# Kernel tuning notes

Hardware: AMD Instinct MI355X
Metric: run time of the kernel (lower is better)

## Reference

```python
import jax, jax.numpy as jnp
import numpy as np

B, T, H = 16, 512, 768
S = 32            # gold spans per example
L = 50            # max_span_len -> candidate ends per span
NT = 3            # num_types
HS = 4 * H        # span repr size


def setup_inputs() -> dict:
    key = jax.random.key(0)
    ks = jax.random.split(key, 8)
    h = jax.random.normal(ks[0], (B, T, H), dtype=jnp.float32)
    attention_mask = jnp.ones((B, T), dtype=jnp.int32)
    starts = jax.random.randint(ks[1], (B, S), 1, 400).astype(jnp.int32)
    lens = jax.random.randint(ks[2], (B, S), 0, L).astype(jnp.int32)
    ends = starts + lens                      # <= 448 < last_tok=510
    types = jax.random.randint(ks[3], (B, S), 0, NT).astype(jnp.int32)
    W1 = jax.random.normal(ks[4], (HS, HS), dtype=jnp.float32) * (1.0 / np.sqrt(HS))
    b1 = jnp.zeros((HS,), dtype=jnp.float32)
    w_score = jax.random.normal(ks[5], (HS,), dtype=jnp.float32) * (1.0 / np.sqrt(HS))
    b_score = jnp.zeros((1,), dtype=jnp.float32)
    W_type = jax.random.normal(ks[6], (HS, NT), dtype=jnp.float32) * (1.0 / np.sqrt(HS))
    b_type = jnp.zeros((NT,), dtype=jnp.float32)
    return {"h": h, "attention_mask": attention_mask, "span_starts": starts,
            "span_ends": ends, "span_types": types, "W1": W1, "b1": b1,
            "w_score": w_score, "b_score": b_score, "W_type": W_type, "b_type": b_type}


def _span_loss(h, attention_mask, span_starts, span_ends, span_types,
               W1, b1, w_score, b_score, W_type, b_type, type_loss_weight=1.0):
    cls = h[:, 0]                                              # [B,H]
    # prefix sums for O(1) segment means: pre[b,t] = sum h[b,0:t]
    pre = jnp.concatenate([jnp.zeros((B, 1, H), h.dtype), jnp.cumsum(h, axis=1)], axis=1)

    valid_len = attention_mask.sum(axis=1)                     # [B]
    last_tok = jnp.maximum(1, valid_len - 2)                   # [B]

    s = span_starts                                            # [B,S]
    e_gold = span_ends
    gold_idx = e_gold - s                                      # [B,S]
    lt = last_tok[:, None]
    span_valid = (s >= 1) & (s <= lt) & (e_gold >= s) & (e_gold <= lt) & (gold_idx < L)

    e_max = jnp.minimum(s + L - 1, lt)                         # [B,S]
    p = s[..., None] + jnp.arange(L, dtype=s.dtype)            # [B,S,L] candidate ends
    cand_valid = p <= e_max[..., None]

    sc = jnp.clip(s, 0, T - 1)
    pc = jnp.clip(p, 0, T - 1)
    bi2 = jnp.arange(B)[:, None]
    bi3 = jnp.arange(B)[:, None, None]

    h_start = h[bi2, sc]                                       # [B,S,H]
    h_end = h[bi3, pc]                                         # [B,S,L,H]
    seg_len = jnp.maximum(p - s[..., None] + 1, 1).astype(h.dtype)
    h_mean = (pre[bi3, pc + 1] - pre[bi2, sc][:, :, None]) / seg_len[..., None]

    repr_ = jnp.concatenate([
        jnp.broadcast_to(h_start[:, :, None], (B, S, L, H)),
        h_end,
        h_mean,
        jnp.broadcast_to(cls[:, None, None], (B, S, L, H)),
    ], axis=-1)                                                # [B,S,L,4H]

    h1 = jax.nn.gelu(jnp.einsum('bslh,hd->bsld', repr_, W1) + b1, approximate=False)
    scores = jnp.einsum('bsld,d->bsl', h1, w_score) + b_score[0]      # [B,S,L]
    type_logits = jnp.einsum('bsld,dk->bslk', h1, W_type) + b_type    # [B,S,L,NT]

    # end-index CE over valid candidate ends
    masked = jnp.where(cand_valid, scores, jnp.float32(-1e9))
    logp_end = jax.nn.log_softmax(masked, axis=-1)             # [B,S,L]
    gi = jnp.clip(gold_idx, 0, L - 1)
    end_loss = -jnp.take_along_axis(logp_end, gi[..., None], axis=-1)[..., 0]  # [B,S]

    # type CE at the gold end index
    tl_gold = jnp.take_along_axis(type_logits, gi[..., None, None], axis=2)[:, :, 0]  # [B,S,NT]
    logp_t = jax.nn.log_softmax(tl_gold, axis=-1)
    tg = jnp.clip(span_types, 0, NT - 1)
    type_loss = -jnp.take_along_axis(logp_t, tg[..., None], axis=-1)[..., 0]  # [B,S]

    vmask = span_valid.astype(h.dtype)
    n_seg = vmask.sum()
    denom = jnp.maximum(n_seg, 1.0)
    loss_end = jnp.where(n_seg > 0, (end_loss * vmask).sum() / denom, 0.0)
    loss_type = jnp.where(n_seg > 0, (type_loss * vmask).sum() / denom, 0.0)
    return loss_end + type_loss_weight * loss_type


def reference(h, attention_mask, span_starts, span_ends, span_types,
              W1, b1, w_score, b_score, W_type, b_type):
    return _span_loss(h, attention_mask, span_starts, span_ends, span_types,
                      W1, b1, w_score, b_score, W_type, b_type)
```

## Files before the change

kernel.cpp:

```cpp
#include <hip/hip_runtime.h>
#include <hip/hip_bf16.h>
#include <math.h>

#define B_ 16
#define T_ 512
#define H_ 768
#define S_ 32
#define L_ 50
#define NT_ 3
#define HS_ 3072
#define CH_ 32
#define CT_ 16

#define TX_ 464
#define YB2 7424
#define GB 14848
#define CLSB 15360
#define XYROWS 14848
#define AROWS 15616
#define NKT 24
#define SLOT_SH 16384

typedef __attribute__((ext_vector_type(8))) short short8;
typedef __attribute__((ext_vector_type(4))) float f32x4;

__device__ __forceinline__ unsigned short f2bf(float f) {
    __hip_bfloat16 b = __float2bfloat16(f);
    return *(unsigned short*)&b;
}
__device__ __forceinline__ float bf2f(unsigned short u) {
    union { unsigned int i; float f; } v; v.i = ((unsigned int)u) << 16; return v.f;
}
__device__ __forceinline__ void load_lds16(const void* g, void* l) {
    __builtin_amdgcn_global_load_lds((__attribute__((address_space(1))) void*)g,
                                     (__attribute__((address_space(3))) void*)l, 16, 0, 0);
}
__device__ __forceinline__ ushort4 pack4(float4 v) {
    ushort4 o; o.x = f2bf(v.x); o.y = f2bf(v.y); o.z = f2bf(v.z); o.w = f2bf(v.w);
    return o;
}

__device__ __forceinline__ float gelu_exact(float v) {
    float a = fabsf(v) * 0.70710678118654752f;
    float t = __builtin_amdgcn_rcpf(fmaf(a, 0.47047f, 1.0f));
    float poly = t * fmaf(t, fmaf(t, 0.7478556f, -0.0958798f), 0.3480242f);
    float e = __builtin_amdgcn_exp2f(a * a * -1.4426950408889634f);
    float erfa = fmaf(-poly, e, 1.0f);
    float erfv = copysignf(erfa, v);
    return 0.5f * v * (1.0f + erfv);
}

__global__ __launch_bounds__(256) void cumsum_pass1(const float4* __restrict__ h4,
                                                    float4* __restrict__ partial) {
    int idx = blockIdx.x * 256 + threadIdx.x;
    int hd4 = idx % 192; int t = idx / 192; int ch = t % CH_; int b = t / CH_;
    const float4* hp = h4 + ((size_t)b * T_ + ch * CT_) * 192 + hd4;
    float4 acc = {0.f, 0.f, 0.f, 0.f};
#pragma unroll
    for (int tt = 0; tt < CT_; tt++) {
        float4 v = hp[(size_t)tt * 192];
        acc.x += v.x; acc.y += v.y; acc.z += v.z; acc.w += v.w;
    }
    partial[idx] = acc;
}

__global__ __launch_bounds__(256) void cumsum_pass3(const float4* __restrict__ h4,
                                                    const float4* __restrict__ partial,
                                                    ushort4* __restrict__ Ab4,
                                                    const float* __restrict__ h,
                                                    const int* __restrict__ starts) {
    if (blockIdx.x >= B_ * CH_ * 192 / 256) {
        int r = blockIdx.x - B_ * CH_ * 192 / 256;
        int src_row, dst_row;
        if (r < B_ * S_) {
            int b = r / S_;
            int sv = starts[r];
            int sc = min(max(sv, 0), T_ - 1);
            src_row = b * T_ + sc;
            dst_row = GB + r;
        } else {
            int b = r - B_ * S_;
            src_row = b * T_;
            dst_row = CLSB + b;
        }
        __hip_bfloat16* dst = (__hip_bfloat16*)Ab4 + (size_t)dst_row * H_;
        const float* src = h + (size_t)src_row * H_;
        for (int j = threadIdx.x; j < H_; j += 256)
            dst[j] = __float2bfloat16(src[j]);
        return;
    }
    int idx = blockIdx.x * 256 + threadIdx.x;
    int hd4 = idx % 192; int t = idx / 192; int ch = t % CH_; int b = t / CH_;
    if (ch * CT_ >= TX_) return;
    float4 acc = {0.f, 0.f, 0.f, 0.f};
#pragma unroll
    for (int c = 0; c < CH_; c++) {
        if (c < ch) {
            float4 v = partial[((size_t)b * CH_ + c) * 192 + hd4];
            acc.x += v.x; acc.y += v.y; acc.z += v.z; acc.w += v.w;
        }
    }
    const float4* hp = h4 + ((size_t)b * T_ + ch * CT_) * 192 + hd4;
    if (ch == 0) {
        ushort4 z = {0, 0, 0, 0};
        Ab4[((size_t)(YB2 + b * TX_)) * 192 + hd4] = z;
    }
#pragma unroll
    for (int tt = 0; tt < CT_; tt++) {
        int t2 = ch * CT_ + tt;
        float4 hv = hp[(size_t)tt * 192];
        if (t2 < TX_)
            Ab4[((size_t)(b * TX_ + t2)) * 192 + hd4] = pack4(hv);
        acc.x += hv.x; acc.y += hv.y; acc.z += hv.z; acc.w += hv.w;
        if (t2 + 1 < TX_)
            Ab4[((size_t)(YB2 + b * TX_ + t2 + 1)) * 192 + hd4] = pack4(acc);
    }
}

__global__ __launch_bounds__(256) void transpose_w(const float* __restrict__ W1,
                                                   __hip_bfloat16* __restrict__ Wt) {
    __shared__ float tile[64][65];
    int n0 = blockIdx.x * 64, k0 = blockIdx.y * 64;
    int c = threadIdx.x & 63, r0 = threadIdx.x >> 6;
#pragma unroll
    for (int i = 0; i < 16; i++) {
        int r = r0 + i * 4;
        tile[r][c] = W1[(size_t)(k0 + r) * HS_ + n0 + c];
    }
    __syncthreads();
    int p = k0 / H_, kl = k0 % H_;
    __hip_bfloat16* out = Wt + (size_t)p * HS_ * H_;
#pragma unroll
    for (int i = 0; i < 16; i++) {
        int r = r0 + i * 4;
        out[(size_t)(n0 + r) * H_ + kl + c] = __float2bfloat16(tile[c][r]);
    }
}

__device__ __forceinline__ void mfma16(const short8 (&a)[4], const short8 (&b)[4],
                                       f32x4 (&acc)[8][4], int off) {
#pragma unroll
    for (int mf = 0; mf < 4; ++mf)
#pragma unroll
        for (int nf = 0; nf < 4; ++nf)
            acc[off + mf][nf] = __builtin_amdgcn_mfma_f32_16x16x32_bf16(
                a[mf], b[nf], acc[off + mf][nf], 0, 0, 0);
}

#define STAGE_A(nslot, k0_) {                                                  \
    char* d_ = (char*)(nslot) + dstoff;                                        \
    load_lds16(pA + (k0_), d_);                                                \
    load_lds16(pA + (size_t)128 * H_ + (k0_), d_ + 8192);                      \
}
#define STAGE_B(nslot, k0_) {                                                  \
    char* d_ = (char*)(nslot) + 16384 + dstoff;                                \
    load_lds16(pB + (k0_), d_);                                                \
    load_lds16(pB + (size_t)128 * H_ + (k0_), d_ + 8192);                      \
}

#define TILE_STEP(kt, WAITSTR, DO_STAGE)                                       \
  {                                                                            \
    const short* slot = lds + ((kt) & 3) * SLOT_SH;                            \
    short* nslot = lds + (((kt) + 3) & 3) * SLOT_SH;                           \
    asm volatile(WAITSTR ::: "memory");                                        \
    __builtin_amdgcn_s_barrier();                                              \
    __builtin_amdgcn_sched_barrier(0);                                         \
    short8 a[4], b[4];                                                         \
    _Pragma("unroll")                                                          \
    for (int i = 0; i < 4; ++i)                                                \
      a[i] = *(const short8*)&slot[(wr * 128 + i * 16 + l15) * 32 + pcs];      \
    _Pragma("unroll")                                                          \
    for (int i = 0; i < 4; ++i)                                                \
      b[i] = *(const short8*)&slot[8192 + (wc * 64 + i * 16 + l15) * 32 + pcs];\
    if (DO_STAGE) { STAGE_A(nslot, ((kt) + 3) * 32) }                          \
    asm volatile("s_waitcnt lgkmcnt(0)" ::: "memory");                         \
    __builtin_amdgcn_sched_barrier(0);                                         \
    __builtin_amdgcn_s_setprio(1);                                             \
    mfma16(a, b, acc, 0);                                                      \
    __builtin_amdgcn_s_setprio(0);                                             \
    __builtin_amdgcn_s_barrier();                                              \
    _Pragma("unroll")                                                          \
    for (int i = 0; i < 4; ++i)                                                \
      a[i] = *(const short8*)&slot[(wr * 128 + 64 + i * 16 + l15) * 32 + pcs]; \
    if (DO_STAGE) { STAGE_B(nslot, ((kt) + 3) * 32) }                          \
    asm volatile("s_waitcnt lgkmcnt(0)" ::: "memory");                         \
    __builtin_amdgcn_sched_barrier(0);                                         \
    __builtin_amdgcn_s_setprio(1);                                             \
    mfma16(a, b, acc, 4);                                                      \
    __builtin_amdgcn_s_setprio(0);                                             \
  }

__global__ __launch_bounds__(512, 2) void mfma_gemm(const __hip_bfloat16* __restrict__ Ab,
                                                    const __hip_bfloat16* __restrict__ Wt,
                                                    __hip_bfloat16* __restrict__ XY,
                                                    float* __restrict__ ST,
                                                    float* __restrict__ CC) {
    __shared__ short lds[4 * SLOT_SH];
    int tid = threadIdx.x;
    int wave = tid >> 6, lane = tid & 63;
    int wr = wave >> 2, wc = wave & 3;
    int l15 = lane & 15;
    int pcs = ((lane >> 4) ^ ((l15 >> 1) & 3)) * 8;

    int orig = blockIdx.x;
    int xcd = orig & 7, loc = orig >> 3;
    int wg = (xcd < 4 ? xcd * 92 : 368 + (xcd - 4) * 91) + loc;
    int mt = wg / 12, nt = wg - mt * 12;
    int m0 = mt << 8, n0 = nt << 8;

    const __hip_bfloat16* Bt;
    if (m0 < YB2)        Bt = Wt + (size_t)1 * HS_ * H_;
    else if (m0 < GB)    Bt = Wt + (size_t)2 * HS_ * H_;
    else if (m0 < CLSB)  Bt = Wt;
    else                 Bt = Wt + (size_t)3 * HS_ * H_;

    int srow = wave * 16 + (lane >> 2);
    int lcS = ((lane & 3) ^ ((lane >> 3) & 3)) * 8;
    const __hip_bfloat16* pA = Ab + (size_t)(m0 + srow) * H_ + lcS;
    const __hip_bfloat16* pB = Bt + (size_t)(n0 + srow) * H_ + lcS;
    int dstoff = wave * 1024;

    f32x4 acc[8][4] = {};

#pragma unroll
    for (int t = 0; t < 3; ++t) {
        STAGE_A(lds + t * SLOT_SH, t * 32)
        STAGE_B(lds + t * SLOT_SH, t * 32)
    }

    for (int kt = 0; kt < NKT - 3; ++kt)
        TILE_STEP(kt, "s_waitcnt vmcnt(8)", true)
    TILE_STEP(NKT - 3, "s_waitcnt vmcnt(8)", false)
    TILE_STEP(NKT - 2, "s_waitcnt vmcnt(4)", false)
    TILE_STEP(NKT - 1, "s_waitcnt vmcnt(0)", false)

    int mb = m0 + wr * 128, nb = n0 + wc * 64;
#pragma unroll
    for (int mf = 0; mf < 8; ++mf) {
#pragma unroll
        for (int nf = 0; nf < 4; ++nf) {
            int n = nb + nf * 16 + l15;
            int mr = mb + mf * 16 + (lane >> 4) * 4;
#pragma unroll
            for (int r = 0; r < 4; ++r) {
                int m = mr + r;
                float v = acc[mf][nf][r];
                if (m < XYROWS) {
                    XY[(size_t)m * HS_ + n] = __float2bfloat16(v);
                } else if (m < CLSB) {
                    ST[(size_t)(m - GB) * HS_ + n] = v;
                } else if (m < CLSB + 16) {
                    CC[(size_t)(m - CLSB) * HS_ + n] = v;
                }
            }
        }
    }
}

__global__ __launch_bounds__(256) void combine_kernel(
    const float* __restrict__ ST, const float* __restrict__ CC,
    const float* __restrict__ b1, const float* __restrict__ w_score,
    const __hip_bfloat16* __restrict__ XY,
    const float* __restrict__ b_score, const float* __restrict__ W_type,
    const int* __restrict__ starts, const int* __restrict__ ends,
    float* __restrict__ scores, float* __restrict__ tgold) {
    int x = blockIdx.x;
    int b = x & 15, s = x >> 4;
    int bs = b * S_ + s;
    int wave = threadIdx.x >> 6, lane = threadIdx.x & 63;
    int sv = starts[bs], ev = ends[bs];
    int gi = min(max(ev - sv, 0), L_ - 1);
    int sc = min(max(sv, 0), TX_ - 1);
    float bs0 = b_score[0];

    union U8 { short8 s; unsigned short u[8]; };
    short8 ysv[6], cv[6], wv[6];
    const unsigned short* Ysr = (const unsigned short*)(XY + (size_t)(YB2 + b * TX_ + sc) * HS_);
    const float* STr = ST + (size_t)bs * HS_;
    const float* CCr = CC + (size_t)b * HS_;
#pragma unroll
    for (int j = 0; j < 6; j++) {
        int d = j * 512 + lane * 8;
        ysv[j] = *(const short8*)(Ysr + d);
        float4 sa = *(const float4*)(STr + d),     sb = *(const float4*)(STr + d + 4);
        float4 ca = *(const float4*)(CCr + d),     cb = *(const float4*)(CCr + d + 4);
        float4 ba = *(const float4*)(b1 + d),      bb = *(const float4*)(b1 + d + 4);
        U8 uc;
        uc.u[0] = f2bf(sa.x + ca.x + ba.x); uc.u[1] = f2bf(sa.y + ca.y + ba.y);
        uc.u[2] = f2bf(sa.z + ca.z + ba.z); uc.u[3] = f2bf(sa.w + ca.w + ba.w);
        uc.u[4] = f2bf(sb.x + cb.x + bb.x); uc.u[5] = f2bf(sb.y + cb.y + bb.y);
        uc.u[6] = f2bf(sb.z + cb.z + bb.z); uc.u[7] = f2bf(sb.w + cb.w + bb.w);
        cv[j] = uc.s;
        float4 wa = *(const float4*)(w_score + d), wb = *(const float4*)(w_score + d + 4);
        U8 uw;
        uw.u[0] = f2bf(wa.x); uw.u[1] = f2bf(wa.y); uw.u[2] = f2bf(wa.z); uw.u[3] = f2bf(wa.w);
        uw.u[4] = f2bf(wb.x); uw.u[5] = f2bf(wb.y); uw.u[6] = f2bf(wb.z); uw.u[7] = f2bf(wb.w);
        wv[j] = uw.s;
    }

    for (int pr = wave; pr < L_ / 2; pr += 4) {
        int l0 = pr * 2, l1 = l0 + 1;
        int pc0 = min(max(sv + l0, 0), TX_ - 2);
        int pc1 = min(max(sv + l1, 0), TX_ - 2);
        float inv0 = 1.0f / (float)(l0 + 1);
        float inv1 = 1.0f / (float)(l1 + 1);
        bool isg0 = (l0 == gi), isg1 = (l1 == gi);
        bool anyg = isg0 || isg1;

        const unsigned short* X0 = (const unsigned short*)(XY + (size_t)(b * TX_ + pc0) * HS_);
        const unsigned short* X1 = (const unsigned short*)(XY + (size_t)(b * TX_ + pc1) * HS_);
        const unsigned short* Y0 = (const unsigned short*)(XY + (size_t)(YB2 + b * TX_ + pc0 + 1) * HS_);
        const unsigned short* Y1 = (const unsigned short*)(XY + (size_t)(YB2 + b * TX_ + pc1 + 1) * HS_);

        float local0 = 0.f, local1 = 0.f, t0 = 0.f, t1 = 0.f, t2 = 0.f;
#pragma unroll
        for (int j = 0; j < 6; j++) {
            int d = j * 512 + lane * 8;
            short8 xv0 = *(const short8*)(X0 + d);
            short8 xv1 = *(const short8*)(X1 + d);
            short8 yv0 = *(const short8*)(Y0 + d);
            short8 yv1 = *(const short8*)(Y1 + d);
#pragma unroll
            for (int q = 0; q < 8; q++) {
                float ys = bf2f(((const unsigned short*)&ysv[j])[q]);
                float cvq = bf2f(((const unsigned short*)&cv[j])[q]);
                float w  = bf2f(((const unsigned short*)&wv[j])[q]);
                float v0 = fmaf(bf2f(((const unsigned short*)&yv0)[q]) - ys, inv0, cvq) +
                           bf2f(((const unsigned short*)&xv0)[q]);
                float v1 = fmaf(bf2f(((const unsigned short*)&yv1)[q]) - ys, inv1, cvq) +
                           bf2f(((const unsigned short*)&xv1)[q]);
                float g0 = gelu_exact(v0);
                float g1 = gelu_exact(v1);
                local0 = fmaf(g0, w, local0);
                local1 = fmaf(g1, w, local1);
                if (anyg) {
                    float gg = isg0 ? g0 : g1;
                    t0 = fmaf(gg, W_type[(d + q) * NT_ + 0], t0);
                    t1 = fmaf(gg, W_type[(d + q) * NT_ + 1], t1);
                    t2 = fmaf(gg, W_type[(d + q) * NT_ + 2], t2);
                }
            }
        }
#pragma unroll
        for (int off = 32; off >= 1; off >>= 1) {
            local0 += __shfl_down(local0, off);
            local1 += __shfl_down(local1, off);
        }
        if (lane == 0) {
            scores[(size_t)bs * L_ + l0] = local0 + bs0;
            scores[(size_t)bs * L_ + l1] = local1 + bs0;
        }
        if (anyg) {
#pragma unroll
            for (int off = 32; off >= 1; off >>= 1) {
                t0 += __shfl_down(t0, off);
                t1 += __shfl_down(t1, off);
                t2 += __shfl_down(t2, off);
            }
            if (lane == 0) {
                tgold[bs * NT_ + 0] = t0;
                tgold[bs * NT_ + 1] = t1;
                tgold[bs * NT_ + 2] = t2;
            }
        }
    }
}

__global__ __launch_bounds__(512) void loss_kernel(
    const float* __restrict__ scores, const float* __restrict__ tgold,
    const int* __restrict__ mask, const int* __restrict__ starts,
    const int* __restrict__ ends, const int* __restrict__ types,
    const float* __restrict__ b_type, float* __restrict__ out) {
    __shared__ int svl[B_];
    __shared__ float r[3][8];
    int tid = threadIdx.x;
    int b = tid / S_;
    if (tid < B_) svl[tid] = 0;
    __syncthreads();
    {
        int part = 0;
        const int* mp = mask + tid * 16;
#pragma unroll
        for (int i = 0; i < 16; i++) part += mp[i];
        atomicAdd(&svl[tid / (T_ / 16)], part);
    }
    __syncthreads();
    int vl = svl[b];
    int lt = max(1, vl - 2);
    int sv = starts[tid], ev = ends[tid];
    int gold = ev - sv;
    bool valid = (sv >= 1) && (sv <= lt) && (ev >= sv) && (ev <= lt) && (gold < L_);
    int emax = min(sv + L_ - 1, lt);
    const float* sp = scores + (size_t)tid * L_;
    float m = -1e30f;
    for (int l = 0; l < L_; l++) {
        float v = (sv + l <= emax) ? sp[l] : -1e9f;
        m = fmaxf(m, v);
    }
    float sum = 0.f;
    for (int l = 0; l < L_; l++) {
        float v = (sv + l <= emax) ? sp[l] : -1e9f;
        sum += expf(v - m);
    }
    int gi = min(max(gold, 0), L_ - 1);
    float vg = (sv + gi <= emax) ? sp[gi] : -1e9f;
    float end_loss = (m + logf(sum)) - vg;

    float t0 = tgold[tid * 3 + 0] + b_type[0];
    float t1 = tgold[tid * 3 + 1] + b_type[1];
    float t2 = tgold[tid * 3 + 2] + b_type[2];
    float tm = fmaxf(t0, fmaxf(t1, t2));
    float tsum = expf(t0 - tm) + expf(t1 - tm) + expf(t2 - tm);
    int tg = min(max(types[tid], 0), NT_ - 1);
    float tv = (tg == 0) ? t0 : ((tg == 1) ? t1 : t2);
    float type_loss = (tm + logf(tsum)) - tv;

    float ve = valid ? end_loss : 0.f;
    float vt = valid ? type_loss : 0.f;
    float vc = valid ? 1.f : 0.f;
    for (int off = 32; off >= 1; off >>= 1) {
        ve += __shfl_down(ve, off);
        vt += __shfl_down(vt, off);
        vc += __shfl_down(vc, off);
    }
    if ((tid & 63) == 0) {
        int w = tid >> 6;
        r[0][w] = ve; r[1][w] = vt; r[2][w] = vc;
    }
    __syncthreads();
    if (tid == 0) {
        float se = 0, st = 0, n = 0;
        for (int w = 0; w < 8; w++) { se += r[0][w]; st += r[1][w]; n += r[2][w]; }
        float denom = fmaxf(n, 1.f);
        out[0] = (n > 0.f) ? (se / denom + st / denom) : 0.f;
    }
}

extern "C" void kernel_launch(void* const* d_in, const int* in_sizes, int n_in,
                              void* d_out, int out_size, void* d_ws, size_t ws_size,
                              hipStream_t stream) {
    const float* h       = (const float*)d_in[0];
    const int*   mask    = (const int*)d_in[1];
    const int*   starts  = (const int*)d_in[2];
    const int*   ends    = (const int*)d_in[3];
    const int*   types   = (const int*)d_in[4];
    const float* W1      = (const float*)d_in[5];
    const float* b1      = (const float*)d_in[6];
    const float* w_score = (const float*)d_in[7];
    const float* b_score = (const float*)d_in[8];
    const float* W_type  = (const float*)d_in[9];
    const float* b_type  = (const float*)d_in[10];
    float* out = (float*)d_out;

    char* ws = (char*)d_ws;
    size_t off = 0;
    __hip_bfloat16* Ab = (__hip_bfloat16*)(ws + off); off += (size_t)AROWS * H_ * 2;
    __hip_bfloat16* XY = (__hip_bfloat16*)(ws + off); off += (size_t)XYROWS * HS_ * 2;
    __hip_bfloat16* Wt = (__hip_bfloat16*)(ws + off); off += (size_t)4 * HS_ * H_ * 2;
    float* ST     = (float*)(ws + off);               off += (size_t)512 * HS_ * 4;
    float* CC     = (float*)(ws + off);               off += (size_t)16 * HS_ * 4;
    float* scores = (float*)(ws + off);               off += (size_t)B_ * S_ * L_ * 4;
    float* tgold  = (float*)(ws + off);               off += (size_t)B_ * S_ * NT_ * 4;
    float4* partial = (float4*)XY;

    hipLaunchKernelGGL(cumsum_pass1, dim3(B_ * CH_ * 192 / 256), dim3(256), 0, stream,
                       (const float4*)h, partial);
    hipLaunchKernelGGL(cumsum_pass3, dim3(B_ * CH_ * 192 / 256 + B_ * S_ + B_), dim3(256),
                       0, stream, (const float4*)h, (const float4*)partial, (ushort4*)Ab,
                       h, starts);
    hipLaunchKernelGGL(transpose_w, dim3(48, 48), dim3(256), 0, stream, W1, Wt);
    hipLaunchKernelGGL(mfma_gemm, dim3((AROWS / 256) * 12), dim3(512), 0, stream,
                       Ab, Wt, XY, ST, CC);
    hipLaunchKernelGGL(combine_kernel, dim3(B_ * S_), dim3(256), 0, stream,
                       ST, CC, b1, w_score, XY, b_score, W_type, starts, ends,
                       scores, tgold);
    hipLaunchKernelGGL(loss_kernel, dim3(1), dim3(512), 0, stream,
                       scores, tgold, mask, starts, ends, types, b_type, out);
}
```

Measured before the change: 371.8 us.

## Split combine kernel over candidate halves and stage span vectors in LDS

The combine kernel now launches twice as many blocks, each handling about half of the 25 candidate-end pairs for one span. The per-span ys/cv/w vectors move from registers into shared memory, and launch bounds plus a smaller unroll are set to cut register pressure. The goal is more occupancy and parallelism in this gather-heavy stage. The cost is that each block redoes the prologue loads and pays an extra barrier and LDS reads per pass.

```diff
diff --git a/kernel.cpp b/kernel.cpp
--- a/kernel.cpp
+++ b/kernel.cpp
@@ -257,48 +257,52 @@
     }
 }
 
-__global__ __launch_bounds__(256) void combine_kernel(
+__global__ __launch_bounds__(256, 4) void combine_kernel(
     const float* __restrict__ ST, const float* __restrict__ CC,
     const float* __restrict__ b1, const float* __restrict__ w_score,
     const __hip_bfloat16* __restrict__ XY,
     const float* __restrict__ b_score, const float* __restrict__ W_type,
     const int* __restrict__ starts, const int* __restrict__ ends,
     float* __restrict__ scores, float* __restrict__ tgold) {
+    __shared__ unsigned short ysL[HS_];
+    __shared__ unsigned short cvL[HS_];
+    __shared__ unsigned short wvL[HS_];
     int x = blockIdx.x;
     int b = x & 15, s = x >> 4;
     int bs = b * S_ + s;
-    int wave = threadIdx.x >> 6, lane = threadIdx.x & 63;
+    int tid = threadIdx.x;
+    int wave = tid >> 6, lane = tid & 63;
     int sv = starts[bs], ev = ends[bs];
     int gi = min(max(ev - sv, 0), L_ - 1);
     int sc = min(max(sv, 0), TX_ - 1);
     float bs0 = b_score[0];
 
-    union U8 { short8 s; unsigned short u[8]; };
-    short8 ysv[6], cv[6], wv[6];
     const unsigned short* Ysr = (const unsigned short*)(XY + (size_t)(YB2 + b * TX_ + sc) * HS_);
     const float* STr = ST + (size_t)bs * HS_;
     const float* CCr = CC + (size_t)b * HS_;
-#pragma unroll
-    for (int j = 0; j < 6; j++) {
-        int d = j * 512 + lane * 8;
-        ysv[j] = *(const short8*)(Ysr + d);
-        float4 sa = *(const float4*)(STr + d),     sb = *(const float4*)(STr + d + 4);
-        float4 ca = *(const float4*)(CCr + d),     cb = *(const float4*)(CCr + d + 4);
-        float4 ba = *(const float4*)(b1 + d),      bb = *(const float4*)(b1 + d + 4);
+    union U8 { short8 s; unsigned short u[8]; };
+    for (int d = tid * 8; d < HS_; d += 2048) {
+        *(short8*)&ysL[d] = *(const short8*)(Ysr + d);
+        float4 sa = *(const float4*)(STr + d), sb = *(const float4*)(STr + d + 4);
+        float4 ca = *(const float4*)(CCr + d), cb = *(const float4*)(CCr + d + 4);
+        float4 ba = *(const float4*)(b1 + d),  bb = *(const float4*)(b1 + d + 4);
         U8 uc;
         uc.u[0] = f2bf(sa.x + ca.x + ba.x); uc.u[1] = f2bf(sa.y + ca.y + ba.y);
         uc.u[2] = f2bf(sa.z + ca.z + ba.z); uc.u[3] = f2bf(sa.w + ca.w + ba.w);
         uc.u[4] = f2bf(sb.x + cb.x + bb.x); uc.u[5] = f2bf(sb.y + cb.y + bb.y);
         uc.u[6] = f2bf(sb.z + cb.z + bb.z); uc.u[7] = f2bf(sb.w + cb.w + bb.w);
-        cv[j] = uc.s;
+        *(short8*)&cvL[d] = uc.s;
         float4 wa = *(const float4*)(w_score + d), wb = *(const float4*)(w_score + d + 4);
         U8 uw;
         uw.u[0] = f2bf(wa.x); uw.u[1] = f2bf(wa.y); uw.u[2] = f2bf(wa.z); uw.u[3] = f2bf(wa.w);
         uw.u[4] = f2bf(wb.x); uw.u[5] = f2bf(wb.y); uw.u[6] = f2bf(wb.z); uw.u[7] = f2bf(wb.w);
-        wv[j] = uw.s;
-    }
-
-    for (int pr = wave; pr < L_ / 2; pr += 4) {
+        *(short8*)&wvL[d] = uw.s;
+    }
+    __syncthreads();
+
+    int lo = blockIdx.y ? 13 : 0;
+    int hi = blockIdx.y ? L_ / 2 : 13;
+    for (int pr = lo + wave; pr < hi; pr += 4) {
         int l0 = pr * 2, l1 = l0 + 1;
         int pc0 = min(max(sv + l0, 0), TX_ - 2);
         int pc1 = min(max(sv + l1, 0), TX_ - 2);
@@ -313,18 +317,21 @@
         const unsigned short* Y1 = (const unsigned short*)(XY + (size_t)(YB2 + b * TX_ + pc1 + 1) * HS_);
 
         float local0 = 0.f, local1 = 0.f, t0 = 0.f, t1 = 0.f, t2 = 0.f;
-#pragma unroll
+#pragma unroll 2
         for (int j = 0; j < 6; j++) {
             int d = j * 512 + lane * 8;
             short8 xv0 = *(const short8*)(X0 + d);
             short8 xv1 = *(const short8*)(X1 + d);
             short8 yv0 = *(const short8*)(Y0 + d);
             short8 yv1 = *(const short8*)(Y1 + d);
+            short8 ys8 = *(const short8*)&ysL[d];
+            short8 cv8 = *(const short8*)&cvL[d];
+            short8 wv8 = *(const short8*)&wvL[d];
 #pragma unroll
             for (int q = 0; q < 8; q++) {
-                float ys = bf2f(((const unsigned short*)&ysv[j])[q]);
-                float cvq = bf2f(((const unsigned short*)&cv[j])[q]);
-                float w  = bf2f(((const unsigned short*)&wv[j])[q]);
+                float ys = bf2f(((const unsigned short*)&ys8)[q]);
+                float cvq = bf2f(((const unsigned short*)&cv8)[q]);
+                float w  = bf2f(((const unsigned short*)&wv8)[q]);
                 float v0 = fmaf(bf2f(((const unsigned short*)&yv0)[q]) - ys, inv0, cvq) +
                            bf2f(((const unsigned short*)&xv0)[q]);
                 float v1 = fmaf(bf2f(((const unsigned short*)&yv1)[q]) - ys, inv1, cvq) +
@@ -471,7 +478,7 @@
     hipLaunchKernelGGL(transpose_w, dim3(48, 48), dim3(256), 0, stream, W1, Wt);
     hipLaunchKernelGGL(mfma_gemm, dim3((AROWS / 256) * 12), dim3(512), 0, stream,
                        Ab, Wt, XY, ST, CC);
-    hipLaunchKernelGGL(combine_kernel, dim3(B_ * S_), dim3(256), 0, stream,
+    hipLaunchKernelGGL(combine_kernel, dim3(B_ * S_, 2), dim3(256), 0, stream,
                        ST, CC, b1, w_score, XY, b_score, W_type, starts, ends,
                        scores, tgold);
     hipLaunchKernelGGL(loss_kernel, dim3(1), dim3(512), 0, stream,
```

Result: faster. 309.7 us (-16.7%).
